# Kernel tuning notes

Measured on AMD Instinct MI355X. Metric: run time of the kernel, lower is better.

## Reference

```python
import jax, jax.numpy as jnp
import numpy as np

B, N, DIM = 2, 16384, 512
H, D = 8, 64          # heads, dim_head
M = 64                # n_global_queries
SC, DC = 64, 64       # context slices, context_dim


def _linear(x, W, b):
    return x @ W.T + b


def setup_inputs() -> dict:
    key = jax.random.key(0)
    ks = jax.random.split(key, 12)
    def w(k, shape, fan_in):
        return jax.random.normal(k, shape, jnp.float32) / np.sqrt(fan_in)
    return {
        "x": jax.random.normal(ks[0], (B, N, DIM), jnp.float32),
        "context": jax.random.normal(ks[1], (B, H, SC, DC), jnp.float32),
        "q_global": jax.random.normal(ks[2], (1, H, M, D), jnp.float32),
        "Wx": w(ks[3], (H * D, DIM), DIM), "bx": jnp.zeros((H * D,), jnp.float32),
        "Wk": w(ks[4], (D, D), D), "bk": jnp.zeros((D,), jnp.float32),
        "Wv": w(ks[5], (D, D), D), "bv": jnp.zeros((D,), jnp.float32),
        "Wcq": w(ks[6], (D, D), D), "bcq": jnp.zeros((D,), jnp.float32),
        "Wck": w(ks[7], (D, DC), DC), "bck": jnp.zeros((D,), jnp.float32),
        "Wcv": w(ks[8], (D, DC), DC), "bcv": jnp.zeros((D,), jnp.float32),
        "state_mixing": jnp.zeros((), jnp.float32),
        "Wo": w(ks[9], (DIM, H * D), H * D), "bo": jnp.zeros((DIM,), jnp.float32),
    }


def reference(x, context, q_global, Wx, bx, Wk, bk, Wv, bv,
              Wcq, bcq, Wck, bck, Wcv, bcv, state_mixing, Wo, bo):
    scale = 1.0  # module uses self.scale = 1.0 (no 1/sqrt(d))
    b, n, _ = x.shape
    # in-projection: (B,N,C) -> (B,H,N,D)
    x_mid = _linear(x, Wx, bx).reshape(b, n, H, D).transpose(0, 2, 1, 3)

    # ---- FLARE low-rank self-attention (routing via M global queries) ----
    k = _linear(x_mid, Wk, bk)  # (B,H,N,D)
    v = _linear(x_mid, Wv, bv)  # (B,H,N,D)
    # encode: global queries attend over N tokens -> latent (B,H,M,D)
    enc = jax.nn.softmax(jnp.einsum('ghmd,bhnd->bhmn', q_global, k) * scale, axis=-1)
    latent = jnp.einsum('bhmn,bhnd->bhmd', enc, v)
    # decode: tokens (keys as queries) attend over M latents -> (B,H,N,D)
    dec = jax.nn.softmax(jnp.einsum('bhnd,ghmd->bhnm', k, q_global) * scale, axis=-1)
    self_attn = jnp.einsum('bhnm,bhmd->bhnd', dec, latent)

    # ---- cross-attention to geometry-aware context ----
    q = _linear(x_mid, Wcq, bcq)          # (B,H,N,D)
    kc = _linear(context, Wck, bck)       # (B,H,Sc,D)
    vc = _linear(context, Wcv, bcv)       # (B,H,Sc,D)
    attn = jax.nn.softmax(jnp.einsum('bhnd,bhsd->bhns', q, kc) * scale, axis=-1)
    cross_attn = jnp.einsum('bhns,bhsd->bhnd', attn, vc)

    # ---- sigmoid-gated mixing ----
    w = jax.nn.sigmoid(state_mixing)
    out = w * self_attn + (1.0 - w) * cross_attn  # (B,H,N,D)

    out = out.transpose(0, 2, 1, 3).reshape(b, n, H * D)
    return _linear(out, Wo, bo)  # (B,N,C); dropout=0 (eval)
```

## Files before the change

### kernel.cpp

```cpp
#include <hip/hip_runtime.h>


typedef unsigned short u16;
typedef __attribute__((ext_vector_type(4))) float  f32x4;
typedef __attribute__((ext_vector_type(4))) u16    u16x4;
typedef __attribute__((ext_vector_type(8))) __bf16 bf16x8;

__device__ __forceinline__ float bf2f(u16 u) {
    return __uint_as_float(((unsigned)u) << 16);
}
__device__ __forceinline__ u16 f2bf(float f) {
    unsigned u = __float_as_uint(f);
    u += 0x7fffu + ((u >> 16) & 1u);
    return (u16)(u >> 16);
}
__device__ __forceinline__ void gload16(const void* g, void* l) {
    __builtin_amdgcn_global_load_lds(
        (const __attribute__((address_space(1))) unsigned int*)g,
        (__attribute__((address_space(3))) unsigned int*)l, 16, 0, 0);
}

#define MASK_NONE 0x7fffffffu

template<int BM, int BN, int WMW, int WNW>
__device__ __forceinline__ void gemm_core(
    const u16* __restrict__ A, int lda, unsigned amask, int koffA,
    const u16* __restrict__ Bm, int ldb, unsigned bmask, int koffB,
    int K, int trow, int tcol,
    u16* As, u16* Bs,
    f32x4 (&acc)[BM / WMW / 16][BN / WNW / 16])
{
    constexpr int FM = BM / WMW / 16;
    constexpr int FN = BN / WNW / 16;
    const int tid  = threadIdx.x;
    const int wid  = tid >> 6, lane = tid & 63;
    const int wm   = wid % WMW, wn = wid / WMW;
    const int wr   = wm * (BM / WMW), wc = wn * (BN / WNW);
    const int lrow = lane & 15, lk = (lane >> 4) * 8;

    for (int kt = 0; kt < K; kt += 32) {
        __syncthreads();
#pragma unroll
        for (int i = 0; i < BM / 64; i++) {
            int c = i * 256 + tid;
            int row = c >> 2, kg = c & 3;
            unsigned kk = ((unsigned)(koffA + kt + kg * 8)) & amask;
            gload16(A + (size_t)(trow + row) * lda + kk, As + (size_t)c * 8);
        }
#pragma unroll
        for (int i = 0; i < BN / 64; i++) {
            int c = i * 256 + tid;
            int col = c >> 2, kg = c & 3;
            unsigned kk = ((unsigned)(koffB + kt + kg * 8)) & bmask;
            gload16(Bm + (size_t)(tcol + col) * ldb + kk, Bs + (size_t)c * 8);
        }
        __syncthreads();

        bf16x8 af[FM], bfr[FN];
#pragma unroll
        for (int fm = 0; fm < FM; fm++)
            af[fm] = *(const bf16x8*)&As[(wr + fm * 16 + lrow) * 32 + lk];
#pragma unroll
        for (int fn = 0; fn < FN; fn++)
            bfr[fn] = *(const bf16x8*)&Bs[(wc + fn * 16 + lrow) * 32 + lk];
#pragma unroll
        for (int fm = 0; fm < FM; fm++)
#pragma unroll
            for (int fn = 0; fn < FN; fn++)
                acc[fm][fn] = __builtin_amdgcn_mfma_f32_16x16x32_bf16(
                    af[fm], bfr[fn], acc[fm][fn], 0, 0, 0);
    }
}


__global__ void prep_x(const float* __restrict__ x, u16* __restrict__ xs)
{
    int t = blockIdx.x * 256 + threadIdx.x;
    int n = t >> 7, e4 = (t & 127) << 2;
    f32x4 v = *(const f32x4*)(x + (size_t)n * 512 + e4);
    u16x4 hi;
#pragma unroll
    for (int j = 0; j < 4; j++) hi[j] = f2bf(v[j]);
    *(u16x4*)(xs + (size_t)n * 512 + e4) = hi;
}

__global__ void prep_w(const float* Wk, const float* Wcq, const float* Wv,
                       const float* Wx, const float* Wo,
                       float* CKF, float* CQF, u16* wV, u16* wo16)
{
    int idx = blockIdx.x * 256 + threadIdx.x;
    int which = idx >> 18;
    int rem = idx & 262143;
    if (which == 3) { wo16[rem] = f2bf(Wo[rem]); return; }
    int c = rem >> 9, e = rem & 511;
    int h = c >> 6, d = c & 63;
    const float* W = which == 0 ? Wk : (which == 1 ? Wcq : Wv);
    float s = 0.f;
#pragma unroll 8
    for (int j = 0; j < 64; j++)
        s += W[d * 64 + j] * Wx[(h * 64 + j) * 512 + e];
    if (which == 0)      CKF[(size_t)c * 512 + e] = s;
    else if (which == 1) CQF[(size_t)c * 512 + e] = s;
    else                 wV [(size_t)c * 512 + e] = f2bf(s);
}

__global__ void prep_bias(const float* Wk, const float* Wcq, const float* Wv,
                          const float* bk, const float* bcq, const float* bv,
                          const float* bx, float* biasKQ, float* biasV)
{
    int t = blockIdx.x * 256 + threadIdx.x;
    if (t < 1024) {
        const float* W  = (t < 512) ? Wk : Wcq;
        const float* bb = (t < 512) ? bk : bcq;
        int c = t & 511; int h = c >> 6, d = c & 63;
        float s = bb[d];
        for (int j = 0; j < 64; j++) s += W[d * 64 + j] * bx[h * 64 + j];
        biasKQ[t] = s;
    } else if (t < 1536) {
        int c = t - 1024; int h = c >> 6, d = c & 63;
        float s = bv[d];
        for (int j = 0; j < 64; j++) s += Wv[d * 64 + j] * bx[h * 64 + j];
        biasV[c] = s;
    }
}

__global__ void prep_ctx(const float* ctx, const float* Wck, const float* bck,
                         const float* Wcv, const float* bcv, const float* smix,
                         float* kcf, u16* vcS)
{
    int t = blockIdx.x * 256 + threadIdx.x;
    int bh = t >> 12, r = t & 4095;
    int s_ = r >> 6, d = r & 63;
    const float* crow = ctx + ((size_t)bh * 64 + s_) * 64;
    float kc = bck[d], vc = bcv[d];
#pragma unroll 8
    for (int e = 0; e < 64; e++) {
        float ce = crow[e];
        kc += ce * Wck[d * 64 + e];
        vc += ce * Wcv[d * 64 + e];
    }
    kcf[(size_t)bh * 4096 + s_ * 64 + d] = kc;
    float w = 1.f / (1.f + __expf(-smix[0]));
    vcS[(size_t)bh * 4096 + d * 64 + (s_ ^ ((d & 7) << 3))] = f2bf((1.f - w) * vc);
}

__global__ void prep_b2(const float* CKF, const float* CQF, const float* qg,
                        const float* kcf, const float* biasKQ, u16* BigB, float* CC)
{
    int idx = blockIdx.x * 256 + threadIdx.x;
    if (idx < 262144) {
        int hm = idx >> 9, e = idx & 511;
        int h = hm >> 6;
        float s = 0.f;
#pragma unroll 8
        for (int d = 0; d < 64; d++)
            s += CKF[(size_t)(h * 64 + d) * 512 + e] * qg[(size_t)hm * 64 + d];
        u16 hi = f2bf(s), lo = f2bf(s - bf2f(hi));
#pragma unroll
        for (int b = 0; b < 2; b++) {
            size_t base = (size_t)b * 1048576 + (size_t)hm * 1024;
            BigB[base + e]       = lo;
            BigB[base + 512 + e] = hi;
        }
    } else if (idx < 786432) {
        int i2 = idx - 262144;
        int r = i2 >> 9, e = i2 & 511;
        int b = r >> 9, hs = r & 511;
        int h = hs >> 6, s_ = hs & 63;
        float s = 0.f;
#pragma unroll 8
        for (int d = 0; d < 64; d++)
            s += CQF[(size_t)(h * 64 + d) * 512 + e]
               * kcf[(size_t)(b * 8 + h) * 4096 + s_ * 64 + d];
        u16 hi = f2bf(s), lo = f2bf(s - bf2f(hi));
        size_t base = (size_t)b * 1048576 + (size_t)(512 + hs) * 1024;
        BigB[base + e]       = lo;
        BigB[base + 512 + e] = hi;
    } else if (idx < 787968) {
        int t = idx - 786432;
        if (t < 512) {
            int h = t >> 6;
            float s = 0.f;
            for (int d = 0; d < 64; d++) s += biasKQ[h * 64 + d] * qg[(size_t)t * 64 + d];
            CC[t] = s; CC[1024 + t] = s;
        } else {
            int j = t - 512;
            int b = j >> 9, hs = j & 511;
            int h = hs >> 6, s_ = hs & 63;
            float s = 0.f;
            for (int d = 0; d < 64; d++)
                s += biasKQ[512 + h * 64 + d]
                   * kcf[(size_t)(b * 8 + h) * 4096 + s_ * 64 + d];
            CC[b * 1024 + 512 + hs] = s;
        }
    }
}

__global__ __launch_bounds__(256, 2) void k_vt(const u16* wV, const u16* xs,
                                               const float* biasV, u16* vT)
{
    __shared__ u16 As[128 * 32], Bs[128 * 32];
    f32x4 acc[4][4] = {};
    int b = blockIdx.z;
    int f = blockIdx.y * gridDim.x + blockIdx.x;
    int w = (f & 7) * 64 + (f >> 3);
    int trow = (w & 3) * 128;
    int tcol = (w >> 2) * 128;
    gemm_core<128, 128, 2, 2>(wV, 512, MASK_NONE, 0,
                              xs + (size_t)b * 8388608, 512, MASK_NONE, 0,
                              512, trow, tcol, As, Bs, acc);
    int tid = threadIdx.x, wid = tid >> 6, lane = tid & 63;
    int wr = (wid & 1) * 64, wc = (wid >> 1) * 64;
    int g = lane >> 4, li = lane & 15;
#pragma unroll
    for (int fm = 0; fm < 4; fm++)
#pragma unroll
        for (int fn = 0; fn < 4; fn++) {
            int col = tcol + wc + fn * 16 + li;
#pragma unroll
            for (int j = 0; j < 4; j++) {
                int a = trow + wr + fm * 16 + g * 4 + j;
                vT[((size_t)b * 512 + a) * 16384 + col] = f2bf(acc[fm][fn][j] + biasV[a]);
            }
        }
}

__global__ void k_Lhalf(const u16* xs, const u16* BigB, const float* CC,
                        int colbase, u16* Pout, float* DD)
{
    __shared__ u16 As[128 * 32], Bs[128 * 32];
    f32x4 acc[4][4] = {};
    int f = blockIdx.x;
    int w = (f & 7) * 128 + (f >> 3);
    int jt = w & 3, nb = w >> 2;
    int b = nb >> 7, ntile = nb & 127;
    int trow = ntile * 128, tcol = colbase + jt * 128;
    gemm_core<128, 128, 2, 2>(xs + (size_t)b * 8388608, 512, 511u, 0,
                              BigB + (size_t)b * 1048576, 1024, MASK_NONE, 0,
                              1024, trow, tcol, As, Bs, acc);
    int tid = threadIdx.x, wid = tid >> 6, lane = tid & 63;
    int wm = wid & 1, wn = wid >> 1;
    int wr = wm * 64, wc = wn * 64;
    int g = lane >> 4, li = lane & 15;
    float cj[4];
#pragma unroll
    for (int fn = 0; fn < 4; fn++) cj[fn] = CC[b * 1024 + tcol + wc + fn * 16 + li];

    int h = jt * 2 + wn;
#pragma unroll
    for (int fm = 0; fm < 4; fm++)
#pragma unroll
        for (int j = 0; j < 4; j++) {
            float ev[4]; float dsum = 0.f;
#pragma unroll
            for (int fn = 0; fn < 4; fn++) {
                ev[fn] = __expf(acc[fm][fn][j] + cj[fn]);
                dsum += ev[fn];
            }
            dsum += __shfl_xor(dsum, 1); dsum += __shfl_xor(dsum, 2);
            dsum += __shfl_xor(dsum, 4); dsum += __shfl_xor(dsum, 8);
            float inv = 1.f / dsum;
            int row = trow + wr + fm * 16 + g * 4 + j;
            size_t pb = ((size_t)b * 16384 + row) * 512 + h * 64;
#pragma unroll
            for (int fn = 0; fn < 4; fn++)
                Pout[pb + fn * 16 + li] = f2bf(ev[fn] * inv);
            if (DD != nullptr && li == 0)
                DD[(size_t)(b * 8 + h) * 16384 + row] = dsum;
        }
}

__global__ void k_dene(const u16* P1n, const float* DD, float* denp)
{
    __shared__ float denL[4][64];
    int blk = blockIdx.x;
    int bh = blk >> 4, c = blk & 15;
    int b = bh >> 3, h = bh & 7;
    int t = threadIdx.x;
    int m = t & 63, r = (t >> 6) & 3;
    float s = 0.f;
    const u16* base = P1n + (size_t)b * 16384 * 512 + h * 64 + m;
    const float* ddb = DD + (size_t)bh * 16384;
    for (int i = 0; i < 256; i++) {
        int n = c * 1024 + i * 4 + r;
        s += bf2f(base[(size_t)n * 512]) * ddb[n];
    }
    denL[r][m] = s;
    __syncthreads();
    if (t < 64)
        denp[(size_t)(b * 512 + h * 64 + t) * 16 + c]
            = denL[0][t] + denL[1][t] + denL[2][t] + denL[3][t];
}

__global__ void k_rden(const float* denp, float* dene)
{
    int t = blockIdx.x * 256 + threadIdx.x;
    if (t < 1024) {
        float s = 0.f;
        const float* p = denp + (size_t)t * 16;
        for (int i = 0; i < 16; i++) s += p[i];
        dene[t] = s;
    }
}

__global__ __launch_bounds__(256, 2) void k_latT(const u16* vT, const u16* P1n,
                                                 const float* DD, float* latp)
{
    __shared__ u16 As[64 * 32], Bs[64 * 32];
    f32x4 acc[2][2] = {};
    int ch = blockIdx.x, bh = blockIdx.z;
    int b = bh >> 3, h = bh & 7;
    int koff = ch * 1024;
    int tid = threadIdx.x, wid = tid >> 6, lane = tid & 63;
    int wr = (wid & 1) * 32, wc = (wid >> 1) * 32;
    int lrow = lane & 15, lk = (lane >> 4) * 8;
    const u16* Avt = vT + (size_t)bh * 64 * 16384;

    for (int kt = 0; kt < 1024; kt += 32) {
        __syncthreads();
        {
            int row = tid >> 2, kg = tid & 3;
            gload16(Avt + (size_t)row * 16384 + koff + kt + kg * 8, As + (size_t)tid * 8);
        }
        {
            int nl = tid & 31, m0 = (tid >> 5) * 8;
            int n = koff + kt + nl;
            const u16* src = P1n + ((size_t)b * 16384 + n) * 512 + h * 64 + m0;
            u16x4 p0 = *(const u16x4*)src;
            u16x4 p1 = *(const u16x4*)(src + 4);
            float ddv = DD[(size_t)bh * 16384 + n];
#pragma unroll
            for (int i = 0; i < 4; i++) {
                int m = m0 + i;
                Bs[m * 32 + (nl ^ ((m & 3) << 3))] = f2bf(bf2f(p0[i]) * ddv);
            }
#pragma unroll
            for (int i = 0; i < 4; i++) {
                int m = m0 + 4 + i;
                Bs[m * 32 + (nl ^ ((m & 3) << 3))] = f2bf(bf2f(p1[i]) * ddv);
            }
        }
        __syncthreads();
        bf16x8 af[2], bfv[2];
#pragma unroll
        for (int fm = 0; fm < 2; fm++)
            af[fm] = *(const bf16x8*)&As[(wr + fm * 16 + lrow) * 32 + lk];
#pragma unroll
        for (int fn = 0; fn < 2; fn++) {
            int m = wc + fn * 16 + lrow;
            bfv[fn] = *(const bf16x8*)&Bs[m * 32 + (lk ^ ((m & 3) << 3))];
        }
#pragma unroll
        for (int fm = 0; fm < 2; fm++)
#pragma unroll
            for (int fn = 0; fn < 2; fn++)
                acc[fm][fn] = __builtin_amdgcn_mfma_f32_16x16x32_bf16(
                    af[fm], bfv[fn], acc[fm][fn], 0, 0, 0);
    }
    float* C = latp + ((size_t)ch * 16 + bh) * 4096;
    int g = lane >> 4, li = lane & 15;
#pragma unroll
    for (int fm = 0; fm < 2; fm++)
#pragma unroll
        for (int fn = 0; fn < 2; fn++)
#pragma unroll
            for (int j = 0; j < 4; j++) {
                int row = wr + fm * 16 + g * 4 + j;
                int col = wc + fn * 16 + li;
                C[row * 64 + col] = acc[fm][fn][j];
            }
}

__global__ void k_latfin(const float* latp, const float* dene, const float* smix,
                         u16* latB)
{
    int t = blockIdx.x * 256 + threadIdx.x;
    int bh = t >> 12, r = t & 4095;
    int m = r & 63;
    float w = 1.f / (1.f + __expf(-smix[0]));
    float s = 0.f;
    for (int c = 0; c < 16; c++) s += latp[((size_t)c * 16 + bh) * 4096 + r];
    int b = bh >> 3, h = bh & 7;
    float lat = s / dene[b * 512 + h * 64 + m];
    latB[(size_t)bh * 4096 + r] = f2bf(w * lat);
}

__global__ __launch_bounds__(256, 2) void k_om(const u16* P1n, const u16* P2n,
                                               const u16* latB, const u16* vcS,
                                               u16* OM)
{
    __shared__ u16 As1[128 * 64], As2[128 * 64], Bs1[64 * 64], Vs[64 * 64];
    int b = blockIdx.z, ntile = blockIdx.x;
    int tid = threadIdx.x, wid = tid >> 6, lane = tid & 63;
    int g = lane >> 4, li = lane & 15;
    int lrow = lane & 15, lk = g * 8;
    for (int h = 0; h < 8; h++) {
        __syncthreads();
#pragma unroll
        for (int i = 0; i < 4; i++) {
            int c = i * 256 + tid;
            int n = c >> 3, m0 = (c & 7) * 8;
            size_t srcoff = ((size_t)b * 16384 + ntile * 128 + n) * 512 + h * 64
                          + (m0 ^ ((n & 7) << 3));
            gload16(P1n + srcoff, As1 + (size_t)c * 8);
            gload16(P2n + srcoff, As2 + (size_t)c * 8);
        }
#pragma unroll
        for (int i = 0; i < 2; i++) {
            int c = i * 256 + tid;
            int d = c >> 3, m0 = (c & 7) * 8;
            gload16(latB + (size_t)(b * 8 + h) * 4096 + d * 64
                         + (m0 ^ ((d & 7) << 3)), Bs1 + (size_t)c * 8);
            gload16(vcS  + (size_t)(b * 8 + h) * 4096 + d * 64 + m0,
                    Vs + (size_t)c * 8);
        }
        __syncthreads();
        f32x4 oacc[2][4] = {};
#pragma unroll
        for (int kt = 0; kt < 64; kt += 32) {
            bf16x8 af[2], bfv[4];
#pragma unroll
            for (int fm = 0; fm < 2; fm++) {
                int r = wid * 32 + fm * 16 + lrow;
                af[fm] = *(const bf16x8*)&As1[r * 64 + ((kt + lk) ^ ((r & 7) << 3))];
            }
#pragma unroll
            for (int fn = 0; fn < 4; fn++) {
                int d = fn * 16 + lrow;
                bfv[fn] = *(const bf16x8*)&Bs1[d * 64 + ((kt + lk) ^ ((d & 7) << 3))];
            }
#pragma unroll
            for (int fm = 0; fm < 2; fm++)
#pragma unroll
                for (int fn = 0; fn < 4; fn++)
                    oacc[fm][fn] = __builtin_amdgcn_mfma_f32_16x16x32_bf16(
                        af[fm], bfv[fn], oacc[fm][fn], 0, 0, 0);
#pragma unroll
            for (int fm = 0; fm < 2; fm++) {
                int r = wid * 32 + fm * 16 + lrow;
                af[fm] = *(const bf16x8*)&As2[r * 64 + ((kt + lk) ^ ((r & 7) << 3))];
            }
#pragma unroll
            for (int fn = 0; fn < 4; fn++) {
                int d = fn * 16 + lrow;
                bfv[fn] = *(const bf16x8*)&Vs[d * 64 + ((kt + lk) ^ ((d & 7) << 3))];
            }
#pragma unroll
            for (int fm = 0; fm < 2; fm++)
#pragma unroll
                for (int fn = 0; fn < 4; fn++)
                    oacc[fm][fn] = __builtin_amdgcn_mfma_f32_16x16x32_bf16(
                        af[fm], bfv[fn], oacc[fm][fn], 0, 0, 0);
        }
#pragma unroll
        for (int fm = 0; fm < 2; fm++)
#pragma unroll
            for (int fn = 0; fn < 4; fn++)
#pragma unroll
                for (int j = 0; j < 4; j++) {
                    int rl = wid * 32 + fm * 16 + g * 4 + j;
                    size_t addr = ((size_t)b * 16384 + ntile * 128 + rl) * 512
                                  + h * 64 + fn * 16 + li;
                    OM[addr] = f2bf(oacc[fm][fn][j]);
                }
    }
}

__global__ __launch_bounds__(256, 2) void k_f(const u16* OM, const u16* wo16,
                                              const float* bo, float* out)
{
    __shared__ u16 As[128 * 32], Bs[128 * 32];
    f32x4 acc[4][4] = {};
    int f = blockIdx.y * gridDim.x + blockIdx.x;
    int w = (f & 7) * 128 + (f >> 3);
    int tcol = (w & 3) * 128, trow = (w >> 2) * 128;
    gemm_core<128, 128, 2, 2>(OM, 512, MASK_NONE, 0, wo16, 512, MASK_NONE, 0,
                              512, trow, tcol, As, Bs, acc);
    int tid = threadIdx.x, wid = tid >> 6, lane = tid & 63;
    int wr = (wid & 1) * 64, wc = (wid >> 1) * 64;
    int g = lane >> 4, li = lane & 15;
#pragma unroll
    for (int fm = 0; fm < 4; fm++)
#pragma unroll
        for (int fn = 0; fn < 4; fn++) {
            int col = tcol + wc + fn * 16 + li;
            float bias = bo[col];
#pragma unroll
            for (int j = 0; j < 4; j++) {
                int row = trow + wr + fm * 16 + g * 4 + j;
                out[(size_t)row * 512 + col] = acc[fm][fn][j] + bias;
            }
        }
}

static const size_t XS_OFF   = 0;
static const size_t OMB_OFF  = 0;
static const size_t P1N_OFF  = 33554432;
static const size_t P2N_OFF  = 67108864;
static const size_t VT_OFF   = 100663296;
static const size_t CKF_OFF  = 134217728;
static const size_t CQF_OFF  = 135266304;
static const size_t WV_OFF   = 136314880;
static const size_t WO_OFF   = 136839168;
static const size_t BIGB_OFF = 137363456;
static const size_t KCF_OFF  = 141557760;
static const size_t VCS_OFF  = 141819904;
static const size_t BKQ_OFF  = 141950976;
static const size_t BV_OFF   = 141955072;
static const size_t CC_OFF   = 141957120;
static const size_t DENP_OFF = 141965312;
static const size_t DENE_OFF = 142030848;
static const size_t DD_OFF   = 142034944;
static const size_t LATP_OFF = 143083520;
static const size_t LATB_OFF = 147277824;

extern "C" void kernel_launch(void* const* d_in, const int* in_sizes, int n_in,
                              void* d_out, int out_size, void* d_ws, size_t ws_size,
                              hipStream_t stream)
{
    const float* x    = (const float*)d_in[0];
    const float* ctx  = (const float*)d_in[1];
    const float* qg   = (const float*)d_in[2];
    const float* Wx   = (const float*)d_in[3];
    const float* bx   = (const float*)d_in[4];
    const float* Wk   = (const float*)d_in[5];
    const float* bk   = (const float*)d_in[6];
    const float* Wv   = (const float*)d_in[7];
    const float* bv   = (const float*)d_in[8];
    const float* Wcq  = (const float*)d_in[9];
    const float* bcq  = (const float*)d_in[10];
    const float* Wck  = (const float*)d_in[11];
    const float* bck  = (const float*)d_in[12];
    const float* Wcv  = (const float*)d_in[13];
    const float* bcv  = (const float*)d_in[14];
    const float* smix = (const float*)d_in[15];
    const float* Wo   = (const float*)d_in[16];
    const float* bo   = (const float*)d_in[17];

    char* ws = (char*)d_ws;
    u16*   xs    = (u16*)  (ws + XS_OFF);
    u16*   OM    = (u16*)  (ws + OMB_OFF);
    u16*   P1n   = (u16*)  (ws + P1N_OFF);
    u16*   P2n   = (u16*)  (ws + P2N_OFF);
    u16*   vT    = (u16*)  (ws + VT_OFF);
    float* CKF   = (float*)(ws + CKF_OFF);
    float* CQF   = (float*)(ws + CQF_OFF);
    u16*   wV    = (u16*)  (ws + WV_OFF);
    u16*   wo16  = (u16*)  (ws + WO_OFF);
    u16*   BigB  = (u16*)  (ws + BIGB_OFF);
    float* kcf   = (float*)(ws + KCF_OFF);
    u16*   vcS   = (u16*)  (ws + VCS_OFF);
    float* biasKQ= (float*)(ws + BKQ_OFF);
    float* biasV = (float*)(ws + BV_OFF);
    float* CC    = (float*)(ws + CC_OFF);
    float* denp  = (float*)(ws + DENP_OFF);
    float* dene  = (float*)(ws + DENE_OFF);
    float* DD    = (float*)(ws + DD_OFF);
    float* latp  = (float*)(ws + LATP_OFF);
    u16*   latB  = (u16*)  (ws + LATB_OFF);

    prep_w   <<< 4096, 256, 0, stream>>>(Wk, Wcq, Wv, Wx, Wo, CKF, CQF, wV, wo16);
    prep_bias<<<    6, 256, 0, stream>>>(Wk, Wcq, Wv, bk, bcq, bv, bx, biasKQ, biasV);
    prep_ctx <<<  256, 256, 0, stream>>>(ctx, Wck, bck, Wcv, bcv, smix, kcf, vcS);
    prep_x   <<<16384, 256, 0, stream>>>(x, xs);
    prep_b2  <<< 3078, 256, 0, stream>>>(CKF, CQF, qg, kcf, biasKQ, BigB, CC);

    k_vt    <<<dim3(128,   4, 2), 256, 0, stream>>>(wV, xs, biasV, vT);
    k_Lhalf <<<1024, 256, 0, stream>>>(xs, BigB, CC, 0,   P1n, DD);
    k_Lhalf <<<1024, 256, 0, stream>>>(xs, BigB, CC, 512, P2n, (float*)nullptr);
    k_dene  <<< 256, 256, 0, stream>>>(P1n, DD, denp);
    k_rden  <<<   4, 256, 0, stream>>>(denp, dene);
    k_latT  <<<dim3( 16,   1, 16), 256, 0, stream>>>(vT, P1n, DD, latp);
    k_latfin<<< 256, 256, 0, stream>>>(latp, dene, smix, latB);
    k_om    <<<dim3(128,   1, 2), 256, 0, stream>>>(P1n, P2n, latB, vcS, OM);
    k_f     <<<dim3(  4, 256, 1), 256, 0, stream>>>(OM, wo16, bo, (float*)d_out);
}
```

Before: 278.1 us.

## Fold latent/context values into output projection, replacing OM and final GEMM with K=1024 GEMM

Precomputes per-batch G = [latB; vcT] composed with Wo, so the output becomes a single GEMM of the combined softmax probabilities P12 (N x 1024) against G. This removes the k_om kernel and the OM intermediate round trip. The two half-width L kernels merge into one launch writing an interleaved P12 buffer. The cost is that the final GEMM's K doubles from 512 to 1024, and a new prep_g kernel is added.

```diff
diff --git a/kernel.cpp b/kernel.cpp
--- a/kernel.cpp
+++ b/kernel.cpp
@@ -85,13 +85,11 @@
 }
 
 __global__ void prep_w(const float* Wk, const float* Wcq, const float* Wv,
-                       const float* Wx, const float* Wo,
-                       float* CKF, float* CQF, u16* wV, u16* wo16)
+                       const float* Wx, float* CKF, float* CQF, u16* wV)
 {
     int idx = blockIdx.x * 256 + threadIdx.x;
     int which = idx >> 18;
     int rem = idx & 262143;
-    if (which == 3) { wo16[rem] = f2bf(Wo[rem]); return; }
     int c = rem >> 9, e = rem & 511;
     int h = c >> 6, d = c & 63;
     const float* W = which == 0 ? Wk : (which == 1 ? Wcq : Wv);
@@ -126,7 +124,7 @@
 
 __global__ void prep_ctx(const float* ctx, const float* Wck, const float* bck,
                          const float* Wcv, const float* bcv, const float* smix,
-                         float* kcf, u16* vcS)
+                         float* kcf, u16* vcT)
 {
     int t = blockIdx.x * 256 + threadIdx.x;
     int bh = t >> 12, r = t & 4095;
@@ -141,7 +139,7 @@
     }
     kcf[(size_t)bh * 4096 + s_ * 64 + d] = kc;
     float w = 1.f / (1.f + __expf(-smix[0]));
-    vcS[(size_t)bh * 4096 + d * 64 + (s_ ^ ((d & 7) << 3))] = f2bf((1.f - w) * vc);
+    vcT[(size_t)bh * 4096 + d * 64 + s_] = f2bf((1.f - w) * vc);
 }
 
 __global__ void prep_b2(const float* CKF, const float* CQF, const float* qg,
@@ -225,16 +223,16 @@
         }
 }
 
-__global__ void k_Lhalf(const u16* xs, const u16* BigB, const float* CC,
-                        int colbase, u16* Pout, float* DD)
+__global__ void k_L(const u16* xs, const u16* BigB, const float* CC,
+                    u16* P12, float* DD)
 {
     __shared__ u16 As[128 * 32], Bs[128 * 32];
     f32x4 acc[4][4] = {};
     int f = blockIdx.x;
-    int w = (f & 7) * 128 + (f >> 3);
-    int jt = w & 3, nb = w >> 2;
+    int w = (f & 7) * 256 + (f >> 3);
+    int jt = w & 7, nb = w >> 3;
     int b = nb >> 7, ntile = nb & 127;
-    int trow = ntile * 128, tcol = colbase + jt * 128;
+    int trow = ntile * 128, tcol = jt * 128;
     gemm_core<128, 128, 2, 2>(xs + (size_t)b * 8388608, 512, 511u, 0,
                               BigB + (size_t)b * 1048576, 1024, MASK_NONE, 0,
                               1024, trow, tcol, As, Bs, acc);
@@ -261,16 +259,16 @@
             dsum += __shfl_xor(dsum, 4); dsum += __shfl_xor(dsum, 8);
             float inv = 1.f / dsum;
             int row = trow + wr + fm * 16 + g * 4 + j;
-            size_t pb = ((size_t)b * 16384 + row) * 512 + h * 64;
+            size_t pb = ((size_t)b * 16384 + row) * 1024 + tcol + wc;
 #pragma unroll
             for (int fn = 0; fn < 4; fn++)
-                Pout[pb + fn * 16 + li] = f2bf(ev[fn] * inv);
-            if (DD != nullptr && li == 0)
+                P12[pb + fn * 16 + li] = f2bf(ev[fn] * inv);
+            if (jt < 4 && li == 0)
                 DD[(size_t)(b * 8 + h) * 16384 + row] = dsum;
         }
 }
 
-__global__ void k_dene(const u16* P1n, const float* DD, float* denp)
+__global__ void k_dene(const u16* P12, const float* DD, float* denp)
 {
     __shared__ float denL[4][64];
     int blk = blockIdx.x;
@@ -279,11 +277,11 @@
     int t = threadIdx.x;
     int m = t & 63, r = (t >> 6) & 3;
     float s = 0.f;
-    const u16* base = P1n + (size_t)b * 16384 * 512 + h * 64 + m;
+    const u16* base = P12 + (size_t)b * 16384 * 1024 + h * 64 + m;
     const float* ddb = DD + (size_t)bh * 16384;
     for (int i = 0; i < 256; i++) {
         int n = c * 1024 + i * 4 + r;
-        s += bf2f(base[(size_t)n * 512]) * ddb[n];
+        s += bf2f(base[(size_t)n * 1024]) * ddb[n];
     }
     denL[r][m] = s;
     __syncthreads();
@@ -303,7 +301,7 @@
     }
 }
 
-__global__ __launch_bounds__(256, 2) void k_latT(const u16* vT, const u16* P1n,
+__global__ __launch_bounds__(256, 2) void k_latT(const u16* vT, const u16* P12,
                                                  const float* DD, float* latp)
 {
     __shared__ u16 As[64 * 32], Bs[64 * 32];
@@ -325,7 +323,7 @@
         {
             int nl = tid & 31, m0 = (tid >> 5) * 8;
             int n = koff + kt + nl;
-            const u16* src = P1n + ((size_t)b * 16384 + n) * 512 + h * 64 + m0;
+            const u16* src = P12 + ((size_t)b * 16384 + n) * 1024 + h * 64 + m0;
             u16x4 p0 = *(const u16x4*)src;
             u16x4 p1 = *(const u16x4*)(src + 4);
             float ddv = DD[(size_t)bh * 16384 + n];
@@ -385,97 +383,35 @@
     latB[(size_t)bh * 4096 + r] = f2bf(w * lat);
 }
 
-__global__ __launch_bounds__(256, 2) void k_om(const u16* P1n, const u16* P2n,
-                                               const u16* latB, const u16* vcS,
-                                               u16* OM)
-{
-    __shared__ u16 As1[128 * 64], As2[128 * 64], Bs1[64 * 64], Vs[64 * 64];
-    int b = blockIdx.z, ntile = blockIdx.x;
-    int tid = threadIdx.x, wid = tid >> 6, lane = tid & 63;
-    int g = lane >> 4, li = lane & 15;
-    int lrow = lane & 15, lk = g * 8;
-    for (int h = 0; h < 8; h++) {
-        __syncthreads();
-#pragma unroll
-        for (int i = 0; i < 4; i++) {
-            int c = i * 256 + tid;
-            int n = c >> 3, m0 = (c & 7) * 8;
-            size_t srcoff = ((size_t)b * 16384 + ntile * 128 + n) * 512 + h * 64
-                          + (m0 ^ ((n & 7) << 3));
-            gload16(P1n + srcoff, As1 + (size_t)c * 8);
-            gload16(P2n + srcoff, As2 + (size_t)c * 8);
-        }
-#pragma unroll
-        for (int i = 0; i < 2; i++) {
-            int c = i * 256 + tid;
-            int d = c >> 3, m0 = (c & 7) * 8;
-            gload16(latB + (size_t)(b * 8 + h) * 4096 + d * 64
-                         + (m0 ^ ((d & 7) << 3)), Bs1 + (size_t)c * 8);
-            gload16(vcS  + (size_t)(b * 8 + h) * 4096 + d * 64 + m0,
-                    Vs + (size_t)c * 8);
-        }
-        __syncthreads();
-        f32x4 oacc[2][4] = {};
-#pragma unroll
-        for (int kt = 0; kt < 64; kt += 32) {
-            bf16x8 af[2], bfv[4];
-#pragma unroll
-            for (int fm = 0; fm < 2; fm++) {
-                int r = wid * 32 + fm * 16 + lrow;
-                af[fm] = *(const bf16x8*)&As1[r * 64 + ((kt + lk) ^ ((r & 7) << 3))];
-            }
-#pragma unroll
-            for (int fn = 0; fn < 4; fn++) {
-                int d = fn * 16 + lrow;
-                bfv[fn] = *(const bf16x8*)&Bs1[d * 64 + ((kt + lk) ^ ((d & 7) << 3))];
-            }
-#pragma unroll
-            for (int fm = 0; fm < 2; fm++)
-#pragma unroll
-                for (int fn = 0; fn < 4; fn++)
-                    oacc[fm][fn] = __builtin_amdgcn_mfma_f32_16x16x32_bf16(
-                        af[fm], bfv[fn], oacc[fm][fn], 0, 0, 0);
-#pragma unroll
-            for (int fm = 0; fm < 2; fm++) {
-                int r = wid * 32 + fm * 16 + lrow;
-                af[fm] = *(const bf16x8*)&As2[r * 64 + ((kt + lk) ^ ((r & 7) << 3))];
-            }
-#pragma unroll
-            for (int fn = 0; fn < 4; fn++) {
-                int d = fn * 16 + lrow;
-                bfv[fn] = *(const bf16x8*)&Vs[d * 64 + ((kt + lk) ^ ((d & 7) << 3))];
-            }
-#pragma unroll
-            for (int fm = 0; fm < 2; fm++)
-#pragma unroll
-                for (int fn = 0; fn < 4; fn++)
-                    oacc[fm][fn] = __builtin_amdgcn_mfma_f32_16x16x32_bf16(
-                        af[fm], bfv[fn], oacc[fm][fn], 0, 0, 0);
-        }
-#pragma unroll
-        for (int fm = 0; fm < 2; fm++)
-#pragma unroll
-            for (int fn = 0; fn < 4; fn++)
-#pragma unroll
-                for (int j = 0; j < 4; j++) {
-                    int rl = wid * 32 + fm * 16 + g * 4 + j;
-                    size_t addr = ((size_t)b * 16384 + ntile * 128 + rl) * 512
-                                  + h * 64 + fn * 16 + li;
-                    OM[addr] = f2bf(oacc[fm][fn][j]);
-                }
-    }
-}
-
-__global__ __launch_bounds__(256, 2) void k_f(const u16* OM, const u16* wo16,
-                                              const float* bo, float* out)
+__global__ void prep_g(const u16* latB, const u16* vcT, const float* Wo, u16* G)
+{
+    int idx = blockIdx.x * 256 + threadIdx.x;
+    int b = idx >> 19;
+    int r = idx & 524287;
+    int e = r >> 10, k = r & 1023;
+    int h = (k >> 6) & 7, dm = k & 63;
+    const u16* src = (k < 512) ? latB : vcT;
+    const float* wrow = Wo + (size_t)e * 512 + h * 64;
+    const u16* sb = src + (size_t)(b * 8 + h) * 4096 + dm;
+    float s = 0.f;
+#pragma unroll 8
+    for (int d = 0; d < 64; d++)
+        s += bf2f(sb[d * 64]) * wrow[d];
+    G[(size_t)b * 524288 + (size_t)e * 1024 + k] = f2bf(s);
+}
+
+__global__ __launch_bounds__(256, 2) void k_fbig(const u16* P12, const u16* G,
+                                                 const float* bo, float* out)
 {
     __shared__ u16 As[128 * 32], Bs[128 * 32];
     f32x4 acc[4][4] = {};
     int f = blockIdx.y * gridDim.x + blockIdx.x;
     int w = (f & 7) * 128 + (f >> 3);
     int tcol = (w & 3) * 128, trow = (w >> 2) * 128;
-    gemm_core<128, 128, 2, 2>(OM, 512, MASK_NONE, 0, wo16, 512, MASK_NONE, 0,
-                              512, trow, tcol, As, Bs, acc);
+    int b = trow >> 14;
+    gemm_core<128, 128, 2, 2>(P12, 1024, MASK_NONE, 0,
+                              G + (size_t)b * 524288, 1024, MASK_NONE, 0,
+                              1024, trow, tcol, As, Bs, acc);
     int tid = threadIdx.x, wid = tid >> 6, lane = tid & 63;
     int wr = (wid & 1) * 64, wc = (wid >> 1) * 64;
     int g = lane >> 4, li = lane & 15;
@@ -494,25 +430,23 @@
 }
 
 static const size_t XS_OFF   = 0;
-static const size_t OMB_OFF  = 0;
-static const size_t P1N_OFF  = 33554432;
-static const size_t P2N_OFF  = 67108864;
+static const size_t P12_OFF  = 33554432;
 static const size_t VT_OFF   = 100663296;
 static const size_t CKF_OFF  = 134217728;
 static const size_t CQF_OFF  = 135266304;
 static const size_t WV_OFF   = 136314880;
-static const size_t WO_OFF   = 136839168;
-static const size_t BIGB_OFF = 137363456;
-static const size_t KCF_OFF  = 141557760;
-static const size_t VCS_OFF  = 141819904;
-static const size_t BKQ_OFF  = 141950976;
-static const size_t BV_OFF   = 141955072;
-static const size_t CC_OFF   = 141957120;
-static const size_t DENP_OFF = 141965312;
-static const size_t DENE_OFF = 142030848;
-static const size_t DD_OFF   = 142034944;
-static const size_t LATP_OFF = 143083520;
-static const size_t LATB_OFF = 147277824;
+static const size_t BIGB_OFF = 136839168;
+static const size_t KCF_OFF  = 141033472;
+static const size_t VCT_OFF  = 141295616;
+static const size_t BKQ_OFF  = 141426688;
+static const size_t BV_OFF   = 141430784;
+static const size_t CC_OFF   = 141432832;
+static const size_t DENP_OFF = 141441024;
+static const size_t DENE_OFF = 141506560;
+static const size_t DD_OFF   = 141510656;
+static const size_t LATP_OFF = 142559232;
+static const size_t LATB_OFF = 146753536;
+static const size_t G_OFF    = 146884608;
 
 extern "C" void kernel_launch(void* const* d_in, const int* in_sizes, int n_in,
                               void* d_out, int out_size, void* d_ws, size_t ws_size,
@@ -539,17 +473,14 @@
 
     char* ws = (char*)d_ws;
     u16*   xs    = (u16*)  (ws + XS_OFF);
-    u16*   OM    = (u16*)  (ws + OMB_OFF);
-    u16*   P1n   = (u16*)  (ws + P1N_OFF);
-    u16*   P2n   = (u16*)  (ws + P2N_OFF);
+    u16*   P12   = (u16*)  (ws + P12_OFF);
     u16*   vT    = (u16*)  (ws + VT_OFF);
     float* CKF   = (float*)(ws + CKF_OFF);
     float* CQF   = (float*)(ws + CQF_OFF);
     u16*   wV    = (u16*)  (ws + WV_OFF);
-    u16*   wo16  = (u16*)  (ws + WO_OFF);
     u16*   BigB  = (u16*)  (ws + BIGB_OFF);
     float* kcf   = (float*)(ws + KCF_OFF);
-    u16*   vcS   = (u16*)  (ws + VCS_OFF);
+    u16*   vcT   = (u16*)  (ws + VCT_OFF);
     float* biasKQ= (float*)(ws + BKQ_OFF);
     float* biasV = (float*)(ws + BV_OFF);
     float* CC    = (float*)(ws + CC_OFF);
@@ -558,20 +489,20 @@
     float* DD    = (float*)(ws + DD_OFF);
     float* latp  = (float*)(ws + LATP_OFF);
     u16*   latB  = (u16*)  (ws + LATB_OFF);
-
-    prep_w   <<< 4096, 256, 0, stream>>>(Wk, Wcq, Wv, Wx, Wo, CKF, CQF, wV, wo16);
+    u16*   G     = (u16*)  (ws + G_OFF);
+
+    prep_w   <<< 3072, 256, 0, stream>>>(Wk, Wcq, Wv, Wx, CKF, CQF, wV);
     prep_bias<<<    6, 256, 0, stream>>>(Wk, Wcq, Wv, bk, bcq, bv, bx, biasKQ, biasV);
-    prep_ctx <<<  256, 256, 0, stream>>>(ctx, Wck, bck, Wcv, bcv, smix, kcf, vcS);
+    prep_ctx <<<  256, 256, 0, stream>>>(ctx, Wck, bck, Wcv, bcv, smix, kcf, vcT);
     prep_x   <<<16384, 256, 0, stream>>>(x, xs);
     prep_b2  <<< 3078, 256, 0, stream>>>(CKF, CQF, qg, kcf, biasKQ, BigB, CC);
 
     k_vt    <<<dim3(128,   4, 2), 256, 0, stream>>>(wV, xs, biasV, vT);
-    k_Lhalf <<<1024, 256, 0, stream>>>(xs, BigB, CC, 0,   P1n, DD);
-    k_Lhalf <<<1024, 256, 0, stream>>>(xs, BigB, CC, 512, P2n, (float*)nullptr);
-    k_dene  <<< 256, 256, 0, stream>>>(P1n, DD, denp);
+    k_L     <<<2048, 256, 0, stream>>>(xs, BigB, CC, P12, DD);
+    k_dene  <<< 256, 256, 0, stream>>>(P12, DD, denp);
     k_rden  <<<   4, 256, 0, stream>>>(denp, dene);
-    k_latT  <<<dim3( 16,   1, 16), 256, 0, stream>>>(vT, P1n, DD, latp);
+    k_latT  <<<dim3( 16,   1, 16), 256, 0, stream>>>(vT, P12, DD, latp);
     k_latfin<<< 256, 256, 0, stream>>>(latp, dene, smix, latB);
-    k_om    <<<dim3(128,   1, 2), 256, 0, stream>>>(P1n, P2n, latB, vcS, OM);
-    k_f     <<<dim3(  4, 256, 1), 256, 0, stream>>>(OM, wo16, bo, (float*)d_out);
-}
+    prep_g  <<<4096, 256, 0, stream>>>(latB, vcT, Wo, G);
+    k_fbig  <<<dim3(  4, 256, 1), 256, 0, stream>>>(P12, G, bo, (float*)d_out);
+}
```

Measured after the change: 283.0 us. Within noise of the previous version (+1.8%).
